# Performance work log

Measured on AMD Instinct MI355X. Metric: run time of the kernel, lower is better.

Reference implementation:

```python
import jax, jax.numpy as jnp
import numpy as np

N = 100000          # total nodes
G = 128             # number of graphs
D_IN, D_H, D_OUT = 512, 1024, 512
E = 1600000         # edges (unused by the math, matches forward signature)


def setup_inputs() -> dict:
    key = jax.random.key(0)
    ks = jax.random.split(key, 9)
    x = jax.random.normal(ks[0], (N, D_IN), dtype=jnp.float32)
    edge_index = jax.random.randint(ks[1], (2, E), 0, N, dtype=jnp.int64)
    # sorted batch ids; guarantee every graph id appears at least once
    batch = jnp.sort(jnp.concatenate([
        jnp.arange(G, dtype=jnp.int64),
        jax.random.randint(ks[2], (N - G,), 0, G, dtype=jnp.int64),
    ]))
    s = 0.02
    W0 = jax.random.normal(ks[3], (D_IN, D_H), dtype=jnp.float32) * s
    b0 = jnp.zeros((D_H,), dtype=jnp.float32)
    W1 = jax.random.normal(ks[4], (D_H, D_H), dtype=jnp.float32) * s
    b1 = jnp.zeros((D_H,), dtype=jnp.float32)
    W2 = jax.random.normal(ks[5], (D_H, D_OUT), dtype=jnp.float32) * s
    b2 = jnp.zeros((D_OUT,), dtype=jnp.float32)
    return {"x": x, "edge_index": edge_index, "batch": batch,
            "W0": W0, "b0": b0, "W1": W1, "b1": b1, "W2": W2, "b2": b2}


def reference(x, edge_index, batch, W0, b0, W1, b1, W2, b2):
    # Linear + ReLU stack (dropout p=0 -> identity in eval). edge_index is unused,
    # matching the original module (its 'GCN' layer is a plain nn.Linear).
    h = jax.nn.relu(x @ W0 + b0)
    h = jax.nn.relu(h @ W1 + b1)
    h = jax.nn.relu(h @ W2 + b2)        # [N, D_OUT]
    # global mean pool per graph: fused segment-sum replaces the per-graph mask loop
    sums = jax.ops.segment_sum(h, batch, num_segments=G)                 # [G, D_OUT]
    counts = jax.ops.segment_sum(jnp.ones((h.shape[0],), h.dtype), batch,
                                 num_segments=G)                          # [G]
    return sums / counts[:, None]
```

## Files before the change

### kernel.cpp

```cpp
#include <hip/hip_runtime.h>
#include <cstdint>
#include <cstddef>

typedef __bf16 bf16x8 __attribute__((ext_vector_type(8)));
typedef float f32x4 __attribute__((ext_vector_type(4)));

__device__ __forceinline__ unsigned short f2bf(float f) {
  unsigned u = __float_as_uint(f);
  u += 0x7fffu + ((u >> 16) & 1u);
  return (unsigned short)(u >> 16);
}
__device__ __forceinline__ float bf2f(unsigned short s) {
  return __uint_as_float(((unsigned)s) << 16);
}

__device__ __forceinline__ void gld_lds16(const void* g, void* l) {
  __builtin_amdgcn_global_load_lds(
      (const __attribute__((address_space(1))) void*)g,
      (__attribute__((address_space(3))) void*)l, 16, 0, 0);
}

#define BARM() do { __builtin_amdgcn_s_barrier(); asm volatile("" ::: "memory"); } while (0)
#define VMCNT(n) asm volatile("s_waitcnt vmcnt(" #n ")" ::: "memory")
#define LGKM0()  do { asm volatile("s_waitcnt lgkmcnt(0)" ::: "memory"); \
                      __builtin_amdgcn_sched_barrier(0); } while (0)

__global__ void transpose_w(const float* __restrict__ w, unsigned short* __restrict__ wt,
                            int K, int N) {
  __shared__ float tile[32][33];
  int nt = N >> 5;
  int bx = blockIdx.x % nt;
  int by = blockIdx.x / nt;
  int tx = threadIdx.x & 31, ty = threadIdx.x >> 5;
#pragma unroll
  for (int r = 0; r < 32; r += 8)
    tile[ty + r][tx] = w[(size_t)(by * 32 + ty + r) * N + bx * 32 + tx];
  __syncthreads();
#pragma unroll
  for (int r = 0; r < 32; r += 8)
    wt[(size_t)(bx * 32 + ty + r) * K + by * 32 + tx] = f2bf(tile[tx][ty + r]);
}

__global__ void cvt_x(const float* __restrict__ x, unsigned short* __restrict__ xb,
                      int rows, int nvalid, int D) {
  size_t total = (size_t)rows * D / 8;
  for (size_t i = (size_t)blockIdx.x * blockDim.x + threadIdx.x; i < total;
       i += (size_t)gridDim.x * blockDim.x) {
    size_t e = i * 8;
    int row = (int)(e / (size_t)D);
    uint4 ov;
    if (row < nvalid) {
      const float4* s = (const float4*)(x + e);
      float4 v0 = s[0], v1 = s[1];
      ov.x = (unsigned)f2bf(v0.x) | ((unsigned)f2bf(v0.y) << 16);
      ov.y = (unsigned)f2bf(v0.z) | ((unsigned)f2bf(v0.w) << 16);
      ov.z = (unsigned)f2bf(v1.x) | ((unsigned)f2bf(v1.y) << 16);
      ov.w = (unsigned)f2bf(v1.z) | ((unsigned)f2bf(v1.w) << 16);
    } else {
      ov.x = ov.y = ov.z = ov.w = 0u;
    }
    *(uint4*)(xb + e) = ov;
  }
}

__device__ __forceinline__ bf16x8 read_frag(const unsigned short* region, int row, int kel) {
  int ke = kel ^ (((row >> 1) & 3) << 3);
  return *(const bf16x8*)(region + row * 32 + ke);
}

__device__ __forceinline__ void stage_half(const unsigned short* gpanel, int K, int kofs,
                                           unsigned short* region, int tid) {
#pragma unroll
  for (int r = 0; r < 2; ++r) {
    int row = r * 128 + (tid >> 2);
    int ke = ((tid & 3) * 8) ^ (((row >> 1) & 3) << 3);
    gld_lds16(gpanel + (size_t)row * K + kofs + ke, region + r * 4096 + tid * 8);
  }
}

#define MFMA16(MB, BV)                                                          \
  do {                                                                          \
    __builtin_amdgcn_s_setprio(1);                                              \
    _Pragma("unroll") for (int mm = 0; mm < 4; ++mm) {                          \
      _Pragma("unroll") for (int nn = 0; nn < 4; ++nn)                          \
        acc[(MB) + mm][nn] = __builtin_amdgcn_mfma_f32_16x16x32_bf16(           \
            av[mm], BV[nn], acc[(MB) + mm][nn], 0, 0, 0);                       \
    }                                                                           \
    __builtin_amdgcn_s_setprio(0);                                              \
  } while (0)

#define GEMM_PREAMBLE_AND_KLOOP()                                               \
  const int tid = threadIdx.x;                                                  \
  const int w = tid >> 6, l = tid & 63;                                         \
  const int wm = w >> 2, wn = w & 3;                                            \
  const int lc = l & 15, lk8 = (l >> 4) * 8;                                    \
  const int nbn = N >> 8;                                                       \
  const int nwg = gridDim.x;                                                    \
  const int q = nwg >> 3, rr = nwg & 7;                                         \
  const int xcd = blockIdx.x & 7, ib = blockIdx.x >> 3;                         \
  const int bswz = (xcd < rr ? xcd * (q + 1) : rr * (q + 1) + (xcd - rr) * q) + ib; \
  const int bm = bswz / nbn, bn = bswz - bm * nbn;                              \
  const unsigned short* Ap = A + (size_t)bm * 256 * K;                          \
  const unsigned short* Bp = Bt + (size_t)bn * 256 * K;                         \
  const int T = K >> 6;                                                         \
  f32x4 acc[8][4] = {};                                                         \
  stage_half(Ap, K, 0, &lds[0][0][0][0][0], tid);                               \
  stage_half(Bp, K, 0, &lds[0][1][0][0][0], tid);                               \
  stage_half(Ap, K, 32, &lds[0][0][1][0][0], tid);                              \
  stage_half(Bp, K, 32, &lds[0][1][1][0][0], tid);                              \
  stage_half(Ap, K, 64, &lds[1][0][0][0][0], tid);                              \
  stage_half(Bp, K, 64, &lds[1][1][0][0][0], tid);                              \
  VMCNT(4);                                                                     \
  BARM();                                                                       \
  for (int t = 0; t < T; ++t) {                                                 \
    const int s = t & 1;                                                        \
    const unsigned short* Ak0 = &lds[s][0][0][0][0];                            \
    const unsigned short* Ak1 = &lds[s][0][1][0][0];                            \
    const unsigned short* Bk0 = &lds[s][1][0][0][0];                            \
    const unsigned short* Bk1 = &lds[s][1][1][0][0];                            \
    unsigned short* nAk1 = &lds[s ^ 1][0][1][0][0];                             \
    unsigned short* nBk1 = &lds[s ^ 1][1][1][0][0];                             \
    unsigned short* cAk0 = &lds[s][0][0][0][0];                                 \
    unsigned short* cBk0 = &lds[s][1][0][0][0];                                 \
    bf16x8 av[4], b0[4], b1[4];                                                 \
    _Pragma("unroll") for (int mm = 0; mm < 4; ++mm)                            \
        av[mm] = read_frag(Ak0, wm * 128 + mm * 16 + lc, lk8);                  \
    _Pragma("unroll") for (int nn = 0; nn < 4; ++nn)                            \
        b0[nn] = read_frag(Bk0, wn * 64 + nn * 16 + lc, lk8);                   \
    if (t + 1 < T) stage_half(Ap, K, (t + 1) * 64 + 32, nAk1, tid);             \
    BARM(); LGKM0(); MFMA16(0, b0); BARM();                                     \
    _Pragma("unroll") for (int mm = 0; mm < 4; ++mm)                            \
        av[mm] = read_frag(Ak0, wm * 128 + (4 + mm) * 16 + lc, lk8);            \
    if (t + 1 < T) stage_half(Bp, K, (t + 1) * 64 + 32, nBk1, tid);             \
    BARM(); LGKM0(); MFMA16(4, b0); BARM();                                     \
    _Pragma("unroll") for (int mm = 0; mm < 4; ++mm)                            \
        av[mm] = read_frag(Ak1, wm * 128 + mm * 16 + lc, lk8);                  \
    _Pragma("unroll") for (int nn = 0; nn < 4; ++nn)                            \
        b1[nn] = read_frag(Bk1, wn * 64 + nn * 16 + lc, lk8);                   \
    if (t + 2 < T) stage_half(Ap, K, (t + 2) * 64, cAk0, tid);                  \
    BARM(); LGKM0(); MFMA16(0, b1); BARM();                                     \
    _Pragma("unroll") for (int mm = 0; mm < 4; ++mm)                            \
        av[mm] = read_frag(Ak1, wm * 128 + (4 + mm) * 16 + lc, lk8);            \
    if (t + 2 < T) { stage_half(Bp, K, (t + 2) * 64, cBk0, tid); VMCNT(4); }    \
    else { VMCNT(0); }                                                          \
    BARM(); LGKM0(); MFMA16(4, b1); BARM();                                     \
  }

__global__ __launch_bounds__(512, 2) void gemm256(
    const unsigned short* __restrict__ A,
    const unsigned short* __restrict__ Bt,
    const float* __restrict__ bias,
    unsigned short* __restrict__ C,
    int N, int K) {
  __shared__ alignas(16) unsigned short lds[2][2][2][256][32];
  GEMM_PREAMBLE_AND_KLOOP();

  unsigned short* eps = &lds[0][0][0][0][0];
  float bv[4];
#pragma unroll
  for (int nn = 0; nn < 4; ++nn) bv[nn] = bias[bn * 256 + wn * 64 + nn * 16 + lc];

#pragma unroll
  for (int r = 0; r < 2; ++r) {
    if (wm == r) {
#pragma unroll
      for (int mm = 0; mm < 8; ++mm) {
#pragma unroll
        for (int nn = 0; nn < 4; ++nn) {
          int lcol = wn * 64 + nn * 16 + lc;
#pragma unroll
          for (int j = 0; j < 4; ++j) {
            int lrow = mm * 16 + (l >> 4) * 4 + j;
            float v = fmaxf(acc[mm][nn][j] + bv[nn], 0.0f);
            eps[lrow * 256 + (lcol ^ (((lrow >> 2) & 3) << 4))] = f2bf(v);
          }
        }
      }
    }
    BARM();
#pragma unroll
    for (int it = 0; it < 8; ++it) {
      int flat = it * 512 + tid;
      int lrow = flat >> 5, cb = flat & 31;
      int ce = (cb * 8) ^ (((lrow >> 2) & 3) << 4);
      uint4 v = *(const uint4*)&eps[lrow * 256 + ce];
      *(uint4*)&C[(size_t)(bm * 256 + r * 128 + lrow) * N + bn * 256 + cb * 8] = v;
    }
    BARM();
  }
}

__global__ __launch_bounds__(512, 2) void gemm_pool(
    const unsigned short* __restrict__ A,
    const unsigned short* __restrict__ Bt,
    const float* __restrict__ bias,
    const int* __restrict__ batch,
    float* __restrict__ part,
    int N, int K, int row0, int Nn) {
  __shared__ alignas(16) unsigned short lds[2][2][2][256][32];
  GEMM_PREAMBLE_AND_KLOOP();

  unsigned short* eps = &lds[0][0][0][0][0];
  int* batchLS = (int*)&lds[1][0][0][0][0];
  if (tid < 256) {
    int grow = row0 + bm * 256 + tid;
    batchLS[tid] = (grow < Nn) ? batch[grow] : -1;
  }
  float bv[4];
#pragma unroll
  for (int nn = 0; nn < 4; ++nn) bv[nn] = bias[bn * 256 + wn * 64 + nn * 16 + lc];

#pragma unroll
  for (int r = 0; r < 2; ++r) {
    if (wm == r) {
#pragma unroll
      for (int mm = 0; mm < 8; ++mm) {
#pragma unroll
        for (int nn = 0; nn < 4; ++nn) {
          int lcol = wn * 64 + nn * 16 + lc;
#pragma unroll
          for (int j = 0; j < 4; ++j) {
            int lrow = mm * 16 + (l >> 4) * 4 + j;
            float v = fmaxf(acc[mm][nn][j] + bv[nn], 0.0f);
            eps[lrow * 256 + (lcol ^ (((lrow >> 2) & 3) << 4))] = f2bf(v);
          }
        }
      }
    }
    BARM();
    {
      int col = tid & 255;
      int half = tid >> 8;
      int gcur = -2;
      float run = 0.f;
      int gcolbase = bn * 256 + col;
      for (int i = 0; i < 64; ++i) {
        int lr = half * 64 + i;
        int g = batchLS[r * 128 + lr];
        if (g != gcur) {
          if (gcur >= 0) atomicAdd(&part[(size_t)gcur * N + gcolbase], run);
          gcur = g; run = 0.f;
        }
        run += bf2f(eps[lr * 256 + (col ^ (((lr >> 2) & 3) << 4))]);
      }
      if (gcur >= 0) atomicAdd(&part[(size_t)gcur * N + gcolbase], run);
    }
    BARM();
  }
}

__global__ void zero_part(float* __restrict__ part, int n) {
  int i = blockIdx.x * blockDim.x + threadIdx.x;
  if (i < n) part[i] = 0.f;
}

__global__ void pool_div(const float* __restrict__ part, const int* __restrict__ batch,
                         float* __restrict__ out, int n, int D, int G) {
  int idx = blockIdx.x * blockDim.x + threadIdx.x;
  if (idx >= G * D) return;
  int g = idx / D;
  int lo, hi;
  { int a = 0, b = n; while (a < b) { int m = (a + b) >> 1; if (batch[m] < g) a = m + 1; else b = m; } lo = a; }
  { int a = lo, b = n; while (a < b) { int m = (a + b) >> 1; if (batch[m] < g + 1) a = m + 1; else b = m; } hi = a; }
  out[idx] = part[idx] / (float)(hi - lo);
}

static inline size_t align256(size_t x) { return (x + 255) & ~(size_t)255; }

extern "C" void kernel_launch(void* const* d_in, const int* in_sizes, int n_in,
                              void* d_out, int out_size, void* d_ws, size_t ws_size,
                              hipStream_t stream) {
  const float* x = (const float*)d_in[0];
  const int* batch = (const int*)d_in[2];
  const float* W0 = (const float*)d_in[3];
  const float* b0 = (const float*)d_in[4];
  const float* W1 = (const float*)d_in[5];
  const float* b1 = (const float*)d_in[6];
  const float* W2 = (const float*)d_in[7];
  const float* b2 = (const float*)d_in[8];
  float* out = (float*)d_out;

  const int Nn = in_sizes[2];
  const int DIN = 512, DH = 1024, DOUT = 512;
  const int G = out_size / DOUT;
  const int Mpad = ((Nn + 255) / 256) * 256;

  uint8_t* p = (uint8_t*)d_ws;
  unsigned short* W0t = (unsigned short*)p; p += align256((size_t)DH * DIN * 2);
  unsigned short* W1t = (unsigned short*)p; p += align256((size_t)DH * DH * 2);
  unsigned short* W2t = (unsigned short*)p; p += align256((size_t)DOUT * DH * 2);
  float* part         = (float*)p;          p += align256((size_t)G * DOUT * 4);
  size_t used = (size_t)(p - (uint8_t*)d_ws);
  size_t avail = ws_size > used ? ws_size - used : 0;
  size_t per_row = (size_t)(DIN + DH + DH) * 2;
  long long chl = (long long)(avail / per_row);
  chl = (chl / 256) * 256;
  int CH = (int)(chl < 256 ? 256 : chl);
  if (CH > Mpad) CH = Mpad;
  unsigned short* xb = (unsigned short*)p; p += align256((size_t)CH * DIN * 2);
  unsigned short* h0 = (unsigned short*)p; p += align256((size_t)CH * DH * 2);
  unsigned short* h1 = (unsigned short*)p; p += align256((size_t)CH * DH * 2);

  zero_part<<<dim3((G * DOUT + 255) / 256), 256, 0, stream>>>(part, G * DOUT);

  transpose_w<<<dim3((DIN / 32) * (DH / 32)), 256, 0, stream>>>(W0, W0t, DIN, DH);
  transpose_w<<<dim3((DH / 32) * (DH / 32)), 256, 0, stream>>>(W1, W1t, DH, DH);
  transpose_w<<<dim3((DH / 32) * (DOUT / 32)), 256, 0, stream>>>(W2, W2t, DH, DOUT);

  for (int off = 0; off < Mpad; off += CH) {
    int rows = Mpad - off; if (rows > CH) rows = CH;
    int nvalid = Nn - off;
    size_t cvt_threads = (size_t)rows * DIN / 8;
    int cvt_blocks = (int)((cvt_threads + 255) / 256);
    if (cvt_blocks > 2048) cvt_blocks = 2048;
    cvt_x<<<dim3(cvt_blocks), 256, 0, stream>>>(x + (size_t)off * DIN, xb, rows, nvalid, DIN);

    gemm256<<<dim3((rows / 256) * (DH / 256)), 512, 0, stream>>>(xb, W0t, b0, h0, DH, DIN);
    gemm256<<<dim3((rows / 256) * (DH / 256)), 512, 0, stream>>>(h0, W1t, b1, h1, DH, DH);
    gemm_pool<<<dim3((rows / 256) * (DOUT / 256)), 512, 0, stream>>>(
        h1, W2t, b2, batch, part, DOUT, DH, off, Nn);
  }

  pool_div<<<dim3((G * DOUT + 255) / 256), 256, 0, stream>>>(part, batch, out, Nn, DOUT, G);
}
```

Baseline: 675.6 us.

## Fuse fp32-to-bf16 input conversion into first-layer GEMM A-tile staging

Result: slower. 693.6 us (+2.7%).

```diff
diff --git a/kernel.cpp b/kernel.cpp
--- a/kernel.cpp
+++ b/kernel.cpp
@@ -1,4 +1,5 @@
 #include <hip/hip_runtime.h>
+#include <hip/hip_bf16.h>
 #include <cstdint>
 #include <cstddef>
 
@@ -41,28 +42,6 @@
     wt[(size_t)(bx * 32 + ty + r) * K + by * 32 + tx] = f2bf(tile[tx][ty + r]);
 }
 
-__global__ void cvt_x(const float* __restrict__ x, unsigned short* __restrict__ xb,
-                      int rows, int nvalid, int D) {
-  size_t total = (size_t)rows * D / 8;
-  for (size_t i = (size_t)blockIdx.x * blockDim.x + threadIdx.x; i < total;
-       i += (size_t)gridDim.x * blockDim.x) {
-    size_t e = i * 8;
-    int row = (int)(e / (size_t)D);
-    uint4 ov;
-    if (row < nvalid) {
-      const float4* s = (const float4*)(x + e);
-      float4 v0 = s[0], v1 = s[1];
-      ov.x = (unsigned)f2bf(v0.x) | ((unsigned)f2bf(v0.y) << 16);
-      ov.y = (unsigned)f2bf(v0.z) | ((unsigned)f2bf(v0.w) << 16);
-      ov.z = (unsigned)f2bf(v1.x) | ((unsigned)f2bf(v1.y) << 16);
-      ov.w = (unsigned)f2bf(v1.z) | ((unsigned)f2bf(v1.w) << 16);
-    } else {
-      ov.x = ov.y = ov.z = ov.w = 0u;
-    }
-    *(uint4*)(xb + e) = ov;
-  }
-}
-
 __device__ __forceinline__ bf16x8 read_frag(const unsigned short* region, int row, int kel) {
   int ke = kel ^ (((row >> 1) & 3) << 3);
   return *(const bf16x8*)(region + row * 32 + ke);
@@ -75,6 +54,40 @@
     int row = r * 128 + (tid >> 2);
     int ke = ((tid & 3) * 8) ^ (((row >> 1) & 3) << 3);
     gld_lds16(gpanel + (size_t)row * K + kofs + ke, region + r * 4096 + tid * 8);
+  }
+}
+
+__device__ __forceinline__ void issue_a(const float* xpanel, int K, int kofs, int tid,
+                                        int lim, float4 (&rv)[4]) {
+#pragma unroll
+  for (int r = 0; r < 2; ++r) {
+    int row = r * 128 + (tid >> 2);
+    int rc = row < lim ? row : 0;
+    int ke = ((tid & 3) * 8) ^ (((row >> 1) & 3) << 3);
+    const float* g = xpanel + (size_t)rc * K + kofs + ke;
+    rv[r * 2] = *(const float4*)g;
+    rv[r * 2 + 1] = *(const float4*)(g + 4);
+  }
+}
+
+__device__ __forceinline__ void commit_a(const float4 (&rv)[4], unsigned short* region,
+                                         int tid, int lim) {
+#pragma unroll
+  for (int r = 0; r < 2; ++r) {
+    int row = r * 128 + (tid >> 2);
+    uint4 o;
+    if (row < lim) {
+      float4 v0 = rv[r * 2], v1 = rv[r * 2 + 1];
+      __hip_bfloat162 p0 = __float22bfloat162_rn(float2{v0.x, v0.y});
+      __hip_bfloat162 p1 = __float22bfloat162_rn(float2{v0.z, v0.w});
+      __hip_bfloat162 p2 = __float22bfloat162_rn(float2{v1.x, v1.y});
+      __hip_bfloat162 p3 = __float22bfloat162_rn(float2{v1.z, v1.w});
+      o.x = *(unsigned*)&p0; o.y = *(unsigned*)&p1;
+      o.z = *(unsigned*)&p2; o.w = *(unsigned*)&p3;
+    } else {
+      o.x = o.y = o.z = o.w = 0u;
+    }
+    *(uint4*)(region + r * 4096 + tid * 8) = o;
   }
 }
 
@@ -146,6 +159,35 @@
     BARM(); LGKM0(); MFMA16(4, b1); BARM();                                     \
   }
 
+#define GEMM_EPILOGUE_STORE(CPTR)                                               \
+  unsigned short* eps = &lds[0][0][0][0][0];                                    \
+  float bv[4];                                                                  \
+  _Pragma("unroll") for (int nn = 0; nn < 4; ++nn)                              \
+      bv[nn] = bias[bn * 256 + wn * 64 + nn * 16 + lc];                         \
+  _Pragma("unroll") for (int r = 0; r < 2; ++r) {                               \
+    if (wm == r) {                                                              \
+      _Pragma("unroll") for (int mm = 0; mm < 8; ++mm) {                        \
+        _Pragma("unroll") for (int nn = 0; nn < 4; ++nn) {                      \
+          int lcol = wn * 64 + nn * 16 + lc;                                    \
+          _Pragma("unroll") for (int j = 0; j < 4; ++j) {                       \
+            int lrow = mm * 16 + (l >> 4) * 4 + j;                              \
+            float v = fmaxf(acc[mm][nn][j] + bv[nn], 0.0f);                     \
+            eps[lrow * 256 + (lcol ^ (((lrow >> 2) & 3) << 4))] = f2bf(v);      \
+          }                                                                     \
+        }                                                                       \
+      }                                                                         \
+    }                                                                           \
+    BARM();                                                                     \
+    _Pragma("unroll") for (int it = 0; it < 8; ++it) {                          \
+      int flat = it * 512 + tid;                                                \
+      int lrow = flat >> 5, cb = flat & 31;                                     \
+      int ce = (cb * 8) ^ (((lrow >> 2) & 3) << 4);                             \
+      uint4 v = *(const uint4*)&eps[lrow * 256 + ce];                           \
+      *(uint4*)&(CPTR)[(size_t)(bm * 256 + r * 128 + lrow) * N + bn * 256 + cb * 8] = v; \
+    }                                                                           \
+    BARM();                                                                     \
+  }
+
 __global__ __launch_bounds__(512, 2) void gemm256(
     const unsigned short* __restrict__ A,
     const unsigned short* __restrict__ Bt,
@@ -154,40 +196,88 @@
     int N, int K) {
   __shared__ alignas(16) unsigned short lds[2][2][2][256][32];
   GEMM_PREAMBLE_AND_KLOOP();
-
-  unsigned short* eps = &lds[0][0][0][0][0];
-  float bv[4];
-#pragma unroll
-  for (int nn = 0; nn < 4; ++nn) bv[nn] = bias[bn * 256 + wn * 64 + nn * 16 + lc];
-
-#pragma unroll
-  for (int r = 0; r < 2; ++r) {
-    if (wm == r) {
-#pragma unroll
-      for (int mm = 0; mm < 8; ++mm) {
-#pragma unroll
-        for (int nn = 0; nn < 4; ++nn) {
-          int lcol = wn * 64 + nn * 16 + lc;
-#pragma unroll
-          for (int j = 0; j < 4; ++j) {
-            int lrow = mm * 16 + (l >> 4) * 4 + j;
-            float v = fmaxf(acc[mm][nn][j] + bv[nn], 0.0f);
-            eps[lrow * 256 + (lcol ^ (((lrow >> 2) & 3) << 4))] = f2bf(v);
-          }
-        }
-      }
-    }
-    BARM();
-#pragma unroll
-    for (int it = 0; it < 8; ++it) {
-      int flat = it * 512 + tid;
-      int lrow = flat >> 5, cb = flat & 31;
-      int ce = (cb * 8) ^ (((lrow >> 2) & 3) << 4);
-      uint4 v = *(const uint4*)&eps[lrow * 256 + ce];
-      *(uint4*)&C[(size_t)(bm * 256 + r * 128 + lrow) * N + bn * 256 + cb * 8] = v;
-    }
-    BARM();
-  }
+  GEMM_EPILOGUE_STORE(C);
+}
+
+__global__ __launch_bounds__(512, 2) void gemm_l0(
+    const float* __restrict__ X,
+    const unsigned short* __restrict__ Bt,
+    const float* __restrict__ bias,
+    unsigned short* __restrict__ C,
+    int N, int K, int row0, int Nn) {
+  __shared__ alignas(16) unsigned short lds[2][2][2][256][32];
+  const int tid = threadIdx.x;
+  const int w = tid >> 6, l = tid & 63;
+  const int wm = w >> 2, wn = w & 3;
+  const int lc = l & 15, lk8 = (l >> 4) * 8;
+  const int nbn = N >> 8;
+  const int nwg = gridDim.x;
+  const int q = nwg >> 3, rr = nwg & 7;
+  const int xcd = blockIdx.x & 7, ib = blockIdx.x >> 3;
+  const int bswz = (xcd < rr ? xcd * (q + 1) : rr * (q + 1) + (xcd - rr) * q) + ib;
+  const int bm = bswz / nbn, bn = bswz - bm * nbn;
+
+  const float* xp = X + (size_t)(row0 + bm * 256) * K;
+  const int lim = Nn - (row0 + bm * 256);
+  const unsigned short* Bp = Bt + (size_t)bn * 256 * K;
+  const int T = K >> 6;
+
+  f32x4 acc[8][4] = {};
+  float4 rA0[4], rA1[4];
+
+  issue_a(xp, K, 0, tid, lim, rA0);
+  issue_a(xp, K, 32, tid, lim, rA1);
+  stage_half(Bp, K, 0, &lds[0][1][0][0][0], tid);
+  stage_half(Bp, K, 32, &lds[0][1][1][0][0], tid);
+  VMCNT(4);
+  commit_a(rA0, &lds[0][0][0][0][0], tid, lim);
+  commit_a(rA1, &lds[0][0][1][0][0], tid, lim);
+  if (T > 1) {
+    issue_a(xp, K, 64, tid, lim, rA0);
+    stage_half(Bp, K, 64, &lds[1][1][0][0][0], tid);
+  }
+  VMCNT(6);
+  LGKM0();
+  BARM();
+
+  for (int t = 0; t < T; ++t) {
+    const int s = t & 1;
+    const unsigned short* Ak0 = &lds[s][0][0][0][0];
+    const unsigned short* Ak1 = &lds[s][0][1][0][0];
+    const unsigned short* Bk0 = &lds[s][1][0][0][0];
+    const unsigned short* Bk1 = &lds[s][1][1][0][0];
+    bf16x8 av[4], b0[4], b1[4];
+
+#pragma unroll
+    for (int mm = 0; mm < 4; ++mm) av[mm] = read_frag(Ak0, wm * 128 + mm * 16 + lc, lk8);
+#pragma unroll
+    for (int nn = 0; nn < 4; ++nn) b0[nn] = read_frag(Bk0, wn * 64 + nn * 16 + lc, lk8);
+    if (t + 1 < T) issue_a(xp, K, (t + 1) * 64 + 32, tid, lim, rA1);
+    if (t + 2 < T) { VMCNT(6); } else { VMCNT(0); }
+    if (t + 1 < T) commit_a(rA0, &lds[s ^ 1][0][0][0][0], tid, lim);
+    BARM(); LGKM0(); MFMA16(0, b0); BARM();
+
+#pragma unroll
+    for (int mm = 0; mm < 4; ++mm) av[mm] = read_frag(Ak0, wm * 128 + (4 + mm) * 16 + lc, lk8);
+    if (t + 1 < T) stage_half(Bp, K, (t + 1) * 64 + 32, &lds[s ^ 1][1][1][0][0], tid);
+    BARM(); LGKM0(); MFMA16(4, b0); BARM();
+
+#pragma unroll
+    for (int mm = 0; mm < 4; ++mm) av[mm] = read_frag(Ak1, wm * 128 + mm * 16 + lc, lk8);
+#pragma unroll
+    for (int nn = 0; nn < 4; ++nn) b1[nn] = read_frag(Bk1, wn * 64 + nn * 16 + lc, lk8);
+    if (t + 2 < T) issue_a(xp, K, (t + 2) * 64, tid, lim, rA0);
+    BARM(); LGKM0(); MFMA16(0, b1); BARM();
+
+#pragma unroll
+    for (int mm = 0; mm < 4; ++mm) av[mm] = read_frag(Ak1, wm * 128 + (4 + mm) * 16 + lc, lk8);
+    if (t + 2 < T) stage_half(Bp, K, (t + 2) * 64, &lds[s][1][0][0][0], tid);
+    if (t + 2 < T) { VMCNT(6); } else { VMCNT(0); }
+    if (t + 1 < T) commit_a(rA1, &lds[s ^ 1][0][1][0][0], tid, lim);
+    BARM(); LGKM0(); MFMA16(4, b1); BARM();
+  }
+
+  GEMM_EPILOGUE_STORE(C);
 }
 
 __global__ __launch_bounds__(512, 2) void gemm_pool(
@@ -292,12 +382,11 @@
   float* part         = (float*)p;          p += align256((size_t)G * DOUT * 4);
   size_t used = (size_t)(p - (uint8_t*)d_ws);
   size_t avail = ws_size > used ? ws_size - used : 0;
-  size_t per_row = (size_t)(DIN + DH + DH) * 2;
+  size_t per_row = (size_t)(DH + DH) * 2;
   long long chl = (long long)(avail / per_row);
   chl = (chl / 256) * 256;
   int CH = (int)(chl < 256 ? 256 : chl);
   if (CH > Mpad) CH = Mpad;
-  unsigned short* xb = (unsigned short*)p; p += align256((size_t)CH * DIN * 2);
   unsigned short* h0 = (unsigned short*)p; p += align256((size_t)CH * DH * 2);
   unsigned short* h1 = (unsigned short*)p; p += align256((size_t)CH * DH * 2);
 
@@ -309,13 +398,9 @@
 
   for (int off = 0; off < Mpad; off += CH) {
     int rows = Mpad - off; if (rows > CH) rows = CH;
-    int nvalid = Nn - off;
-    size_t cvt_threads = (size_t)rows * DIN / 8;
-    int cvt_blocks = (int)((cvt_threads + 255) / 256);
-    if (cvt_blocks > 2048) cvt_blocks = 2048;
-    cvt_x<<<dim3(cvt_blocks), 256, 0, stream>>>(x + (size_t)off * DIN, xb, rows, nvalid, DIN);
-
-    gemm256<<<dim3((rows / 256) * (DH / 256)), 512, 0, stream>>>(xb, W0t, b0, h0, DH, DIN);
+
+    gemm_l0<<<dim3((rows / 256) * (DH / 256)), 512, 0, stream>>>(
+        x, W0t, b0, h0, DH, DIN, off, Nn);
     gemm256<<<dim3((rows / 256) * (DH / 256)), 512, 0, stream>>>(h0, W1t, b1, h1, DH, DH);
     gemm_pool<<<dim3((rows / 256) * (DOUT / 256)), 512, 0, stream>>>(
         h1, W2t, b2, batch, part, DOUT, DH, off, Nn);
```

## Use 16-wave 1024-thread blocks with smaller per-wave MFMA tiles in GEMMs

Applied to the files above, without the earlier changes.

After: 659.3 us. -2.4%, faster.

```diff
diff --git a/kernel.cpp b/kernel.cpp
--- a/kernel.cpp
+++ b/kernel.cpp
@@ -70,18 +70,15 @@
 
 __device__ __forceinline__ void stage_half(const unsigned short* gpanel, int K, int kofs,
                                            unsigned short* region, int tid) {
-#pragma unroll
-  for (int r = 0; r < 2; ++r) {
-    int row = r * 128 + (tid >> 2);
-    int ke = ((tid & 3) * 8) ^ (((row >> 1) & 3) << 3);
-    gld_lds16(gpanel + (size_t)row * K + kofs + ke, region + r * 4096 + tid * 8);
-  }
-}
-
-#define MFMA16(MB, BV)                                                          \
+  int row = tid >> 2;
+  int ke = ((tid & 3) * 8) ^ (((row >> 1) & 3) << 3);
+  gld_lds16(gpanel + (size_t)row * K + kofs + ke, region + tid * 8);
+}
+
+#define MFMA8(MB, BV)                                                           \
   do {                                                                          \
     __builtin_amdgcn_s_setprio(1);                                              \
-    _Pragma("unroll") for (int mm = 0; mm < 4; ++mm) {                          \
+    _Pragma("unroll") for (int mm = 0; mm < 2; ++mm) {                          \
       _Pragma("unroll") for (int nn = 0; nn < 4; ++nn)                          \
         acc[(MB) + mm][nn] = __builtin_amdgcn_mfma_f32_16x16x32_bf16(           \
             av[mm], BV[nn], acc[(MB) + mm][nn], 0, 0, 0);                       \
@@ -103,14 +100,14 @@
   const unsigned short* Ap = A + (size_t)bm * 256 * K;                          \
   const unsigned short* Bp = Bt + (size_t)bn * 256 * K;                         \
   const int T = K >> 6;                                                         \
-  f32x4 acc[8][4] = {};                                                         \
+  f32x4 acc[4][4] = {};                                                         \
   stage_half(Ap, K, 0, &lds[0][0][0][0][0], tid);                               \
   stage_half(Bp, K, 0, &lds[0][1][0][0][0], tid);                               \
   stage_half(Ap, K, 32, &lds[0][0][1][0][0], tid);                              \
   stage_half(Bp, K, 32, &lds[0][1][1][0][0], tid);                              \
   stage_half(Ap, K, 64, &lds[1][0][0][0][0], tid);                              \
   stage_half(Bp, K, 64, &lds[1][1][0][0][0], tid);                              \
-  VMCNT(4);                                                                     \
+  VMCNT(2);                                                                     \
   BARM();                                                                       \
   for (int t = 0; t < T; ++t) {                                                 \
     const int s = t & 1;                                                        \
@@ -122,31 +119,35 @@
     unsigned short* nBk1 = &lds[s ^ 1][1][1][0][0];                             \
     unsigned short* cAk0 = &lds[s][0][0][0][0];                                 \
     unsigned short* cBk0 = &lds[s][1][0][0][0];                                 \
-    bf16x8 av[4], b0[4], b1[4];                                                 \
-    _Pragma("unroll") for (int mm = 0; mm < 4; ++mm)                            \
-        av[mm] = read_frag(Ak0, wm * 128 + mm * 16 + lc, lk8);                  \
+    bf16x8 av[2], b0[4], b1[4];                                                 \
+                                    \
+    _Pragma("unroll") for (int mm = 0; mm < 2; ++mm)                            \
+        av[mm] = read_frag(Ak0, wm * 64 + mm * 16 + lc, lk8);                   \
     _Pragma("unroll") for (int nn = 0; nn < 4; ++nn)                            \
         b0[nn] = read_frag(Bk0, wn * 64 + nn * 16 + lc, lk8);                   \
     if (t + 1 < T) stage_half(Ap, K, (t + 1) * 64 + 32, nAk1, tid);             \
-    BARM(); LGKM0(); MFMA16(0, b0); BARM();                                     \
-    _Pragma("unroll") for (int mm = 0; mm < 4; ++mm)                            \
-        av[mm] = read_frag(Ak0, wm * 128 + (4 + mm) * 16 + lc, lk8);            \
+    BARM(); LGKM0(); MFMA8(0, b0); BARM();                                      \
+                                           \
+    _Pragma("unroll") for (int mm = 0; mm < 2; ++mm)                            \
+        av[mm] = read_frag(Ak0, wm * 64 + (2 + mm) * 16 + lc, lk8);             \
     if (t + 1 < T) stage_half(Bp, K, (t + 1) * 64 + 32, nBk1, tid);             \
-    BARM(); LGKM0(); MFMA16(4, b0); BARM();                                     \
-    _Pragma("unroll") for (int mm = 0; mm < 4; ++mm)                            \
-        av[mm] = read_frag(Ak1, wm * 128 + mm * 16 + lc, lk8);                  \
+    BARM(); LGKM0(); MFMA8(2, b0); BARM();                                      \
+                                    \
+    _Pragma("unroll") for (int mm = 0; mm < 2; ++mm)                            \
+        av[mm] = read_frag(Ak1, wm * 64 + mm * 16 + lc, lk8);                   \
     _Pragma("unroll") for (int nn = 0; nn < 4; ++nn)                            \
         b1[nn] = read_frag(Bk1, wn * 64 + nn * 16 + lc, lk8);                   \
     if (t + 2 < T) stage_half(Ap, K, (t + 2) * 64, cAk0, tid);                  \
-    BARM(); LGKM0(); MFMA16(0, b1); BARM();                                     \
-    _Pragma("unroll") for (int mm = 0; mm < 4; ++mm)                            \
-        av[mm] = read_frag(Ak1, wm * 128 + (4 + mm) * 16 + lc, lk8);            \
-    if (t + 2 < T) { stage_half(Bp, K, (t + 2) * 64, cBk0, tid); VMCNT(4); }    \
+    BARM(); LGKM0(); MFMA8(0, b1); BARM();                                      \
+                          \
+    _Pragma("unroll") for (int mm = 0; mm < 2; ++mm)                            \
+        av[mm] = read_frag(Ak1, wm * 64 + (2 + mm) * 16 + lc, lk8);             \
+    if (t + 2 < T) { stage_half(Bp, K, (t + 2) * 64, cBk0, tid); VMCNT(2); }    \
     else { VMCNT(0); }                                                          \
-    BARM(); LGKM0(); MFMA16(4, b1); BARM();                                     \
-  }
-
-__global__ __launch_bounds__(512, 2) void gemm256(
+    BARM(); LGKM0(); MFMA8(2, b1); BARM();                                      \
+  }
+
+__global__ __launch_bounds__(1024, 1) void gemm256(
     const unsigned short* __restrict__ A,
     const unsigned short* __restrict__ Bt,
     const float* __restrict__ bias,
@@ -162,15 +163,15 @@
 
 #pragma unroll
   for (int r = 0; r < 2; ++r) {
-    if (wm == r) {
-#pragma unroll
-      for (int mm = 0; mm < 8; ++mm) {
+    if ((wm >> 1) == r) {
+#pragma unroll
+      for (int mm = 0; mm < 4; ++mm) {
 #pragma unroll
         for (int nn = 0; nn < 4; ++nn) {
           int lcol = wn * 64 + nn * 16 + lc;
 #pragma unroll
           for (int j = 0; j < 4; ++j) {
-            int lrow = mm * 16 + (l >> 4) * 4 + j;
+            int lrow = (wm & 1) * 64 + mm * 16 + (l >> 4) * 4 + j;
             float v = fmaxf(acc[mm][nn][j] + bv[nn], 0.0f);
             eps[lrow * 256 + (lcol ^ (((lrow >> 2) & 3) << 4))] = f2bf(v);
           }
@@ -179,8 +180,8 @@
     }
     BARM();
 #pragma unroll
-    for (int it = 0; it < 8; ++it) {
-      int flat = it * 512 + tid;
+    for (int it = 0; it < 4; ++it) {
+      int flat = it * 1024 + tid;
       int lrow = flat >> 5, cb = flat & 31;
       int ce = (cb * 8) ^ (((lrow >> 2) & 3) << 4);
       uint4 v = *(const uint4*)&eps[lrow * 256 + ce];
@@ -190,7 +191,7 @@
   }
 }
 
-__global__ __launch_bounds__(512, 2) void gemm_pool(
+__global__ __launch_bounds__(1024, 1) void gemm_pool(
     const unsigned short* __restrict__ A,
     const unsigned short* __restrict__ Bt,
     const float* __restrict__ bias,
@@ -212,15 +213,15 @@
 
 #pragma unroll
   for (int r = 0; r < 2; ++r) {
-    if (wm == r) {
-#pragma unroll
-      for (int mm = 0; mm < 8; ++mm) {
+    if ((wm >> 1) == r) {
+#pragma unroll
+      for (int mm = 0; mm < 4; ++mm) {
 #pragma unroll
         for (int nn = 0; nn < 4; ++nn) {
           int lcol = wn * 64 + nn * 16 + lc;
 #pragma unroll
           for (int j = 0; j < 4; ++j) {
-            int lrow = mm * 16 + (l >> 4) * 4 + j;
+            int lrow = (wm & 1) * 64 + mm * 16 + (l >> 4) * 4 + j;
             float v = fmaxf(acc[mm][nn][j] + bv[nn], 0.0f);
             eps[lrow * 256 + (lcol ^ (((lrow >> 2) & 3) << 4))] = f2bf(v);
           }
@@ -230,12 +231,12 @@
     BARM();
     {
       int col = tid & 255;
-      int half = tid >> 8;
+      int qt = tid >> 8;
       int gcur = -2;
       float run = 0.f;
       int gcolbase = bn * 256 + col;
-      for (int i = 0; i < 64; ++i) {
-        int lr = half * 64 + i;
+      for (int i = 0; i < 32; ++i) {
+        int lr = qt * 32 + i;
         int g = batchLS[r * 128 + lr];
         if (g != gcur) {
           if (gcur >= 0) atomicAdd(&part[(size_t)gcur * N + gcolbase], run);
@@ -315,9 +316,9 @@
     if (cvt_blocks > 2048) cvt_blocks = 2048;
     cvt_x<<<dim3(cvt_blocks), 256, 0, stream>>>(x + (size_t)off * DIN, xb, rows, nvalid, DIN);
 
-    gemm256<<<dim3((rows / 256) * (DH / 256)), 512, 0, stream>>>(xb, W0t, b0, h0, DH, DIN);
-    gemm256<<<dim3((rows / 256) * (DH / 256)), 512, 0, stream>>>(h0, W1t, b1, h1, DH, DH);
-    gemm_pool<<<dim3((rows / 256) * (DOUT / 256)), 512, 0, stream>>>(
+    gemm256<<<dim3((rows / 256) * (DH / 256)), 1024, 0, stream>>>(xb, W0t, b0, h0, DH, DIN);
+    gemm256<<<dim3((rows / 256) * (DH / 256)), 1024, 0, stream>>>(h0, W1t, b1, h1, DH, DH);
+    gemm_pool<<<dim3((rows / 256) * (DOUT / 256)), 1024, 0, stream>>>(
         h1, W2t, b2, batch, part, DOUT, DH, off, Nn);
   }
 
```
